# Kernel optimization log

Measured on AMD Instinct MI355X. Metric: run time of the kernel, lower is better.

The kernel has to match this reference:

```python
import jax, jax.numpy as jnp
import numpy as np

# Bahdanau additive attention (eval mode: dropout is identity):
#   fac1 = W @ k        [B, d, S]
#   fac2 = U @ q        [B, d, S]
#   s    = v^T tanh(fac1 + fac2)   [B, 1, S]
#   attn = softmax(s, axis=-1)

B, D, S = 32, 1024, 2048


def setup_inputs() -> dict:
    key = jax.random.key(0)
    kq, kk, kv, kW, kU = jax.random.split(key, 5)
    scale = 1.0 / np.sqrt(D)
    return {
        "q": jax.random.normal(kq, (B, D, S), dtype=jnp.float32),
        "k": jax.random.normal(kk, (B, D, S), dtype=jnp.float32),
        "v": jax.random.normal(kv, (B, D, 1), dtype=jnp.float32),
        "W": jax.random.normal(kW, (D, D), dtype=jnp.float32) * scale,
        "U": jax.random.normal(kU, (D, D), dtype=jnp.float32) * scale,
    }


def reference(q, k, v, W, U):
    # projections: [d,e] x [b,e,s] -> [b,d,s]
    fac1 = jnp.einsum("de,bes->bds", W, k)
    fac2 = jnp.einsum("de,bes->bds", U, q)
    e = jnp.tanh(fac1 + fac2)            # [B, D, S]
    s = jnp.einsum("bdo,bds->bos", v, e)  # [B, 1, S]
    attn = jax.nn.softmax(s, axis=-1)     # softmax over sequence
    return attn
```

## Files before the change

### kernel.cpp

```cpp
#include <hip/hip_runtime.h>

#define D_ 1024
#define S_ 2048
#define B_ 32
#define BM 256
#define BN 256
#define BK 64
#define NKT 32

typedef __attribute__((ext_vector_type(8))) _Float16 f16x8;
typedef __attribute__((ext_vector_type(16))) float f32x16;

__device__ __forceinline__ void async_ld16(const void* g, void* l) {
  __builtin_amdgcn_global_load_lds(
      (const __attribute__((address_space(1))) void*)g,
      (__attribute__((address_space(3))) void*)l, 16, 0, 0);
}

__global__ void prep_kernel(const float* __restrict__ W, const float* __restrict__ U,
                            _Float16* __restrict__ wf, _Float16* __restrict__ uf) {
  int t = blockIdx.x * blockDim.x + threadIdx.x;
  const float* src = blockIdx.y ? U : W;
  _Float16* dst = blockIdx.y ? uf : wf;

  int tile = t >> 11;
  int g    = t & 2047;
  int top  = g >> 6;
  int ks = top >> 3, wr = (top >> 2) & 1, fm = top & 3;
  int lane = g & 63, l31 = lane & 31, lhi = lane >> 5;
  int row   = wr * 128 + fm * 32 + l31;
  int chunk = ks * 2 + lhi;
  int d = (tile >> 4) * 256 + row;
  int e = (tile & 15) * 64 + chunk * 8;

  const float* p = src + (size_t)d * D_ + e;
  f16x8 hv;
#pragma unroll
  for (int j = 0; j < 8; ++j) hv[j] = (_Float16)p[j];
  *(f16x8*)(dst + (size_t)t * 8) = hv;
}

__global__ void __launch_bounds__(512, 2)
gemm_kernel(const float* __restrict__ kten, const float* __restrict__ qten,
            const float* __restrict__ v,
            const _Float16* __restrict__ wf, const _Float16* __restrict__ uf,
            float* __restrict__ partials) {
  __shared__ __align__(16) _Float16 Af[2][BM * BK];
  __shared__ __align__(16) _Float16 Bf[2][BN * BK];
  __shared__ float vbuf[BM];
  __shared__ float red[2][BN];

  const int tid  = threadIdx.x;
  const int lane = tid & 63;
  const int wid  = tid >> 6;
  const int wr   = wid >> 2;
  const int wc   = wid & 3;

  int bid  = blockIdx.x;
  int g    = ((bid >> 5) << 3) | (bid & 7);
  int dblk = (bid >> 3) & 3;
  int st   = g & 7;
  int b    = g >> 3;
  int s0   = st * BN;

  if (tid < BM) vbuf[tid] = v[(size_t)b * D_ + dblk * BM + tid];

  f32x16 acc[4][2];
#pragma unroll
  for (int i = 0; i < 4; ++i)
#pragma unroll
    for (int j = 0; j < 2; ++j)
#pragma unroll
      for (int r = 0; r < 16; ++r) acc[i][j][r] = 0.0f;

  const int nB = tid & 255;
  const int kq = tid >> 8;

  auto writeBhalf = [&](const float* xv, int h, int buf) {
#pragma unroll
    for (int cl = 2 * h; cl < 2 * h + 2; ++cl) {
      f16x8 hv;
#pragma unroll
      for (int w = 0; w < 8; ++w) hv[w] = (_Float16)xv[cl * 8 + w];
      int c = kq * 4 + cl, cks = c >> 1, clh = c & 1;
      int gnl = ((cks * 8 + (nB >> 6) * 2 + ((nB >> 5) & 1)) << 6) | (clh << 5) | (nB & 31);
      *(f16x8*)&Bf[buf][(size_t)gnl * 8] = hv;
    }
  };

  float xv[32];
  {
    const _Float16* at0 = wf + (size_t)(dblk * 16) * 16384;
#pragma unroll
    for (int i = 0; i < 4; ++i)
      async_ld16(at0 + (size_t)(tid + i * 512) * 8, &Af[0][(size_t)(tid + i * 512) * 8]);
    const float* col = kten + (size_t)b * (D_ * S_) + s0 + nB + (size_t)(kq * 32) * S_;
#pragma unroll
    for (int j = 0; j < 32; ++j) xv[j] = col[(size_t)j * S_];
    writeBhalf(xv, 0, 0);
    writeBhalf(xv, 1, 0);
  }
  __syncthreads();

  int cur = 0;
  for (int kt = 0; kt < NKT; ++kt) {
    const int nxt = cur ^ 1;
    const int ktn = (kt + 1 < NKT) ? kt + 1 : kt;
    const int halfn = ktn >> 4, kttn = ktn & 15;
    const _Float16* at_n = (halfn ? uf : wf) + (size_t)(dblk * 16 + kttn) * 16384;
    const float* coln = (halfn ? qten : kten) + (size_t)b * (D_ * S_)
                        + (size_t)(kttn * 64) * S_ + s0 + nB + (size_t)(kq * 32) * S_;

#pragma unroll
    for (int ks = 0; ks < 4; ++ks) {
      if (ks == 0) {
        async_ld16(at_n + (size_t)tid * 8,         &Af[nxt][(size_t)tid * 8]);
        async_ld16(at_n + (size_t)(tid + 512) * 8, &Af[nxt][(size_t)(tid + 512) * 8]);
#pragma unroll
        for (int j = 0; j < 16; ++j) xv[j] = coln[(size_t)j * S_];
      } else if (ks == 1) {
        async_ld16(at_n + (size_t)(tid + 1024) * 8, &Af[nxt][(size_t)(tid + 1024) * 8]);
        async_ld16(at_n + (size_t)(tid + 1536) * 8, &Af[nxt][(size_t)(tid + 1536) * 8]);
#pragma unroll
        for (int j = 16; j < 32; ++j) xv[j] = coln[(size_t)j * S_];
      } else if (ks == 2) {
        writeBhalf(xv, 0, nxt);
      } else {
        writeBhalf(xv, 1, nxt);
      }

      f16x8 af[4], bf[2];
#pragma unroll
      for (int fm = 0; fm < 4; ++fm) {
        int gA = ((ks * 8 + wr * 4 + fm) << 6) + lane;
        af[fm] = *(const f16x8*)&Af[cur][(size_t)gA * 8];
      }
#pragma unroll
      for (int fn = 0; fn < 2; ++fn) {
        int gB = ((ks * 8 + wc * 2 + fn) << 6) + lane;
        bf[fn] = *(const f16x8*)&Bf[cur][(size_t)gB * 8];
      }
      __builtin_amdgcn_s_setprio(1);
#pragma unroll
      for (int fm = 0; fm < 4; ++fm)
#pragma unroll
        for (int fn = 0; fn < 2; ++fn)
          acc[fm][fn] = __builtin_amdgcn_mfma_f32_32x32x16_f16(af[fm], bf[fn], acc[fm][fn], 0, 0, 0);
      __builtin_amdgcn_s_setprio(0);
      if (ks < 3) __builtin_amdgcn_s_barrier();
    }
    __syncthreads();
    cur = nxt;
  }

  float psum[2] = {0.f, 0.f};
#pragma unroll
  for (int fm = 0; fm < 4; ++fm)
#pragma unroll
    for (int fn = 0; fn < 2; ++fn)
#pragma unroll
      for (int r = 0; r < 16; ++r) {
        int row = wr * 128 + fm * 32 + (r & 3) + 8 * (r >> 2) + 4 * (lane >> 5);
        float x  = acc[fm][fn][r];
        float th = 1.0f - 2.0f / (__expf(2.0f * x) + 1.0f);
        psum[fn] += vbuf[row] * th;
      }
#pragma unroll
  for (int fn = 0; fn < 2; ++fn) psum[fn] += __shfl_xor(psum[fn], 32);
  if (lane < 32) {
    red[wr][wc * 64 + lane]      = psum[0];
    red[wr][wc * 64 + 32 + lane] = psum[1];
  }
  __syncthreads();
  if (tid < BN) {
    float val = red[0][tid] + red[1][tid];
    partials[(size_t)(dblk * B_ + b) * S_ + s0 + tid] = val;
  }
}

__global__ void softmax_kernel(const float* __restrict__ partials, float* __restrict__ out) {
  __shared__ float logit[S_];
  __shared__ float wred[2][4];
  int b = blockIdx.x, tid = threadIdx.x;
  int lane = tid & 63, wid = tid >> 6;
  float lmax = -1e30f;
  for (int i = tid; i < S_; i += 256) {
    float acc = 0.f;
#pragma unroll
    for (int d = 0; d < 4; ++d) acc += partials[(size_t)(d * B_ + b) * S_ + i];
    logit[i] = acc;
    lmax = fmaxf(lmax, acc);
  }
#pragma unroll
  for (int o = 32; o; o >>= 1) lmax = fmaxf(lmax, __shfl_xor(lmax, o));
  if (lane == 0) wred[0][wid] = lmax;
  __syncthreads();
  float m = fmaxf(fmaxf(wred[0][0], wred[0][1]), fmaxf(wred[0][2], wred[0][3]));
  float lsum = 0.f;
  for (int i = tid; i < S_; i += 256) {
    float ex = __expf(logit[i] - m);
    logit[i] = ex;
    lsum += ex;
  }
#pragma unroll
  for (int o = 32; o; o >>= 1) lsum += __shfl_xor(lsum, o);
  if (lane == 0) wred[1][wid] = lsum;
  __syncthreads();
  float tot = wred[1][0] + wred[1][1] + wred[1][2] + wred[1][3];
  float inv = 1.0f / tot;
  for (int i = tid; i < S_; i += 256) out[(size_t)b * S_ + i] = logit[i] * inv;
}

extern "C" void kernel_launch(void* const* d_in, const int* in_sizes, int n_in,
                              void* d_out, int out_size, void* d_ws, size_t ws_size,
                              hipStream_t stream) {
  const float* q = (const float*)d_in[0];
  const float* k = (const float*)d_in[1];
  const float* v = (const float*)d_in[2];
  const float* W = (const float*)d_in[3];
  const float* U = (const float*)d_in[4];

  _Float16* wf = (_Float16*)d_ws;
  _Float16* uf = wf + (size_t)D_ * D_;
  float* partials = (float*)(uf + (size_t)D_ * D_);

  prep_kernel<<<dim3(512, 2), 256, 0, stream>>>(W, U, wf, uf);
  gemm_kernel<<<dim3(1024), 512, 0, stream>>>(k, q, v, wf, uf, partials);
  softmax_kernel<<<dim3(B_), 256, 0, stream>>>(partials, (float*)d_out);
}
```

Measured before the change: 460.7 us.

## Deepen B-operand register prefetch to two k-tiles with manual vmcnt waits

Restructures the GEMM main loop so the fp32 k/q global loads run two k-tiles ahead into alternating register buffers (xvA/xvB), while the f16 conversion and LDS write of the previous tile happen in the last phase. An explicit s_waitcnt vmcnt(32) lets the newest 32 global loads stay in flight across the barrier, and the loop is unrolled by two with macros plus a peeled epilogue. This is meant to hide global-load latency for the strided B loads behind more MFMA work. The cost is doubled register usage for the staging buffers under launch_bounds(512,2), which may cause spills, plus reliance on a hand-counted vmcnt value being correct.

```diff
diff --git a/kernel.cpp b/kernel.cpp
--- a/kernel.cpp
+++ b/kernel.cpp
@@ -76,82 +76,95 @@
   const int nB = tid & 255;
   const int kq = tid >> 8;
 
-  auto writeBhalf = [&](const float* xv, int h, int buf) {
-#pragma unroll
-    for (int cl = 2 * h; cl < 2 * h + 2; ++cl) {
-      f16x8 hv;
-#pragma unroll
-      for (int w = 0; w < 8; ++w) hv[w] = (_Float16)xv[cl * 8 + w];
-      int c = kq * 4 + cl, cks = c >> 1, clh = c & 1;
-      int gnl = ((cks * 8 + (nB >> 6) * 2 + ((nB >> 5) & 1)) << 6) | (clh << 5) | (nB & 31);
-      *(f16x8*)&Bf[buf][(size_t)gnl * 8] = hv;
-    }
-  };
-
-  float xv[32];
-  {
-    const _Float16* at0 = wf + (size_t)(dblk * 16) * 16384;
-#pragma unroll
-    for (int i = 0; i < 4; ++i)
-      async_ld16(at0 + (size_t)(tid + i * 512) * 8, &Af[0][(size_t)(tid + i * 512) * 8]);
-    const float* col = kten + (size_t)b * (D_ * S_) + s0 + nB + (size_t)(kq * 32) * S_;
-#pragma unroll
-    for (int j = 0; j < 32; ++j) xv[j] = col[(size_t)j * S_];
-    writeBhalf(xv, 0, 0);
-    writeBhalf(xv, 1, 0);
-  }
-  __syncthreads();
-
-  int cur = 0;
-  for (int kt = 0; kt < NKT; ++kt) {
-    const int nxt = cur ^ 1;
-    const int ktn = (kt + 1 < NKT) ? kt + 1 : kt;
-    const int halfn = ktn >> 4, kttn = ktn & 15;
-    const _Float16* at_n = (halfn ? uf : wf) + (size_t)(dblk * 16 + kttn) * 16384;
-    const float* coln = (halfn ? qten : kten) + (size_t)b * (D_ * S_)
-                        + (size_t)(kttn * 64) * S_ + s0 + nB + (size_t)(kq * 32) * S_;
-
-#pragma unroll
-    for (int ks = 0; ks < 4; ++ks) {
-      if (ks == 0) {
-        async_ld16(at_n + (size_t)tid * 8,         &Af[nxt][(size_t)tid * 8]);
-        async_ld16(at_n + (size_t)(tid + 512) * 8, &Af[nxt][(size_t)(tid + 512) * 8]);
-#pragma unroll
-        for (int j = 0; j < 16; ++j) xv[j] = coln[(size_t)j * S_];
-      } else if (ks == 1) {
-        async_ld16(at_n + (size_t)(tid + 1024) * 8, &Af[nxt][(size_t)(tid + 1024) * 8]);
-        async_ld16(at_n + (size_t)(tid + 1536) * 8, &Af[nxt][(size_t)(tid + 1536) * 8]);
-#pragma unroll
-        for (int j = 16; j < 32; ++j) xv[j] = coln[(size_t)j * S_];
-      } else if (ks == 2) {
-        writeBhalf(xv, 0, nxt);
-      } else {
-        writeBhalf(xv, 1, nxt);
-      }
-
-      f16x8 af[4], bf[2];
-#pragma unroll
-      for (int fm = 0; fm < 4; ++fm) {
-        int gA = ((ks * 8 + wr * 4 + fm) << 6) + lane;
-        af[fm] = *(const f16x8*)&Af[cur][(size_t)gA * 8];
-      }
-#pragma unroll
-      for (int fn = 0; fn < 2; ++fn) {
-        int gB = ((ks * 8 + wc * 2 + fn) << 6) + lane;
-        bf[fn] = *(const f16x8*)&Bf[cur][(size_t)gB * 8];
-      }
-      __builtin_amdgcn_s_setprio(1);
-#pragma unroll
-      for (int fm = 0; fm < 4; ++fm)
-#pragma unroll
-        for (int fn = 0; fn < 2; ++fn)
-          acc[fm][fn] = __builtin_amdgcn_mfma_f32_32x32x16_f16(af[fm], bf[fn], acc[fm][fn], 0, 0, 0);
-      __builtin_amdgcn_s_setprio(0);
-      if (ks < 3) __builtin_amdgcn_s_barrier();
-    }
-    __syncthreads();
-    cur = nxt;
-  }
+#define PH_FENCE asm volatile("" ::: "memory")
+#define PH_BAR __builtin_amdgcn_s_barrier()
+
+#define GLLA(ktn, buf, part) do {                                              \
+    const int half_ = (ktn) >> 4, ktt_ = (ktn) & 15;                           \
+    const _Float16* at_ = (half_ ? uf : wf) + (size_t)(dblk * 16 + ktt_) * 16384; \
+    async_ld16(at_ + (size_t)(tid + (part) * 1024) * 8,                        \
+               &Af[buf][(size_t)(tid + (part) * 1024) * 8]);                   \
+    async_ld16(at_ + (size_t)(tid + (part) * 1024 + 512) * 8,                  \
+               &Af[buf][(size_t)(tid + (part) * 1024 + 512) * 8]);             \
+  } while (0)
+
+#define LOADB(ktn, xv, h) do {                                                 \
+    const int half_ = (ktn) >> 4, ktt_ = (ktn) & 15;                           \
+    const float* col_ = (half_ ? qten : kten) + (size_t)b * (D_ * S_)          \
+                        + (size_t)(ktt_ * 64) * S_ + s0 + nB                   \
+                        + (size_t)(kq * 32) * S_;                              \
+    _Pragma("unroll")                                                          \
+    for (int j = 16 * (h); j < 16 * (h) + 16; ++j) xv[j] = col_[(size_t)j * S_]; \
+  } while (0)
+
+#define CVTWRITE(xv, buf) do {                                                 \
+    _Pragma("unroll")                                                          \
+    for (int cl = 0; cl < 4; ++cl) {                                           \
+      f16x8 hv_;                                                               \
+      _Pragma("unroll")                                                        \
+      for (int w = 0; w < 8; ++w) hv_[w] = (_Float16)xv[cl * 8 + w];           \
+      int c_ = kq * 4 + cl, cks_ = c_ >> 1, clh_ = c_ & 1;                     \
+      int gnl_ = ((cks_ * 8 + (nB >> 6) * 2 + ((nB >> 5) & 1)) << 6)           \
+                 | (clh_ << 5) | (nB & 31);                                    \
+      *(f16x8*)&Bf[buf][(size_t)gnl_ * 8] = hv_;                               \
+    }                                                                          \
+  } while (0)
+
+#define COMPUTE_PHASE(cur_, ks_) do {                                          \
+    f16x8 af_[4], bf_[2];                                                      \
+    _Pragma("unroll")                                                          \
+    for (int fm = 0; fm < 4; ++fm)                                             \
+      af_[fm] = *(const f16x8*)&Af[cur_][(size_t)(((ks_) * 8 + wr * 4 + fm) * 64 + lane) * 8]; \
+    _Pragma("unroll")                                                          \
+    for (int fn = 0; fn < 2; ++fn)                                             \
+      bf_[fn] = *(const f16x8*)&Bf[cur_][(size_t)(((ks_) * 8 + wc * 2 + fn) * 64 + lane) * 8]; \
+    __builtin_amdgcn_s_setprio(1);                                             \
+    _Pragma("unroll")                                                          \
+    for (int fm = 0; fm < 4; ++fm)                                             \
+      _Pragma("unroll")                                                        \
+      for (int fn = 0; fn < 2; ++fn)                                           \
+        acc[fm][fn] = __builtin_amdgcn_mfma_f32_32x32x16_f16(af_[fm], bf_[fn], acc[fm][fn], 0, 0, 0); \
+    __builtin_amdgcn_s_setprio(0);                                             \
+  } while (0)
+
+#define STEP(kt_, cur_, xvC_, xvN_) do {                                       \
+    const int nxt_ = (cur_) ^ 1;                                               \
+    PH_FENCE; GLLA((kt_) + 1, nxt_, 0); COMPUTE_PHASE(cur_, 0); PH_BAR;        \
+    PH_FENCE; GLLA((kt_) + 1, nxt_, 1); COMPUTE_PHASE(cur_, 1); PH_BAR;        \
+    PH_FENCE; LOADB((kt_) + 2, xvN_, 0); COMPUTE_PHASE(cur_, 2); PH_BAR;       \
+    PH_FENCE; LOADB((kt_) + 2, xvN_, 1); CVTWRITE(xvC_, nxt_);                 \
+              COMPUTE_PHASE(cur_, 3);                                          \
+    asm volatile("s_waitcnt vmcnt(32) lgkmcnt(0)" ::: "memory");               \
+    PH_BAR;                                                                    \
+    __builtin_amdgcn_sched_barrier(0);                                         \
+  } while (0)
+
+  float xvA[32], xvB[32];
+  LOADB(0, xvA, 0); LOADB(0, xvA, 1);
+  GLLA(0, 0, 0);    GLLA(0, 0, 1);
+  LOADB(1, xvB, 0); LOADB(1, xvB, 1);
+  CVTWRITE(xvA, 0);
+  __syncthreads();
+
+  for (int it = 0; it < 15; ++it) {
+    STEP(2 * it,     0, xvB, xvA);
+    STEP(2 * it + 1, 1, xvA, xvB);
+  }
+
+  PH_FENCE; GLLA(31, 1, 0); COMPUTE_PHASE(0, 0); PH_BAR;
+  PH_FENCE; GLLA(31, 1, 1); COMPUTE_PHASE(0, 1); PH_BAR;
+  PH_FENCE; COMPUTE_PHASE(0, 2); PH_BAR;
+  PH_FENCE; CVTWRITE(xvB, 1); COMPUTE_PHASE(0, 3);
+  __syncthreads();
+  COMPUTE_PHASE(1, 0); COMPUTE_PHASE(1, 1); COMPUTE_PHASE(1, 2); COMPUTE_PHASE(1, 3);
+
+#undef STEP
+#undef COMPUTE_PHASE
+#undef CVTWRITE
+#undef LOADB
+#undef GLLA
+#undef PH_BAR
+#undef PH_FENCE
 
   float psum[2] = {0.f, 0.f};
 #pragma unroll
```

New measurement: 401.3 us. -12.9%, faster.
